# Optimization experiments

Hardware: AMD Instinct MI355X
Metric: run time of the kernel (lower is better)

The kernel has to match this reference:

```python
import jax, jax.numpy as jnp
import numpy as np
from jax import lax

NH = 8        # num_heads
C = 256       # embedding_dim
WS = 5        # window_size
DN = ('NCHW', 'OIHW', 'NCHW')


def setup_inputs() -> dict:
    key = jax.random.key(0)
    ks = jax.random.split(key, 6)
    B, H, W = 16, 64, 64
    hd = C // NH  # per-head dim = pos_embed_dim
    return {
        "src": jax.random.normal(ks[0], (B, C, H, W), jnp.float32),
        "rel_pos_embed": jax.random.normal(ks[1], (hd, WS, WS), jnp.float32) * 0.02,
        "qkv_w": jax.random.normal(ks[2], (3 * C, C), jnp.float32) * (C ** -0.5),
        "cpe_w": jax.random.normal(ks[3], (C, C, 3, 3), jnp.float32) * (1.0 / np.sqrt(C * 9)),
        "cpe_b": jnp.zeros((C,), jnp.float32),
        "out_w": jax.random.normal(ks[4], (C, C), jnp.float32) * (C ** -0.5),
        "out_b": jnp.zeros((C,), jnp.float32),
    }


def reference(src, rel_pos_embed, qkv_w, cpe_w, cpe_b, out_w, out_b):
    B, Cc, H, W = src.shape
    hd = Cc // NH
    scale = hd ** -0.5

    # conv positional encoding (3x3 conv) + residual
    x = lax.conv_general_dilated(src, cpe_w, (1, 1), [(1, 1), (1, 1)],
                                 dimension_numbers=DN) + cpe_b[None, :, None, None] + src

    # 1x1 qkv conv as a GEMM over channels
    qkv = jnp.einsum('oc,bchw->bohw', qkv_w, x)
    q, k, v = jnp.split(qkv, 3, axis=1)
    q = q.reshape(B * NH, hd, H, W)
    k = k.reshape(B * NH, hd, H, W)
    v = v.reshape(B * NH, hd, H, W)

    # linear (lambda) attention: softmax over spatial positions of k
    kf = jax.nn.softmax(k.reshape(B * NH, hd, H * W), axis=-1)   # (b' i n)
    vf = v.reshape(B * NH, hd, H * W)                            # (b' o n)
    content_lambda = jnp.einsum('bin,bon->bio', kf, vf)          # (b' i o), tiny
    qf = q.reshape(B * NH, hd, H * W) * scale
    content = jnp.einsum('bin,bio->bon', qf, content_lambda).reshape(B * NH, hd, H, W)

    # depthwise conv positional lambda on v
    pad = WS // 2
    pos_lambda = lax.conv_general_dilated(v, rel_pos_embed[:, None], (1, 1),
                                          [(pad, pad), (pad, pad)],
                                          dimension_numbers=DN,
                                          feature_group_count=hd)
    result = (content + q * pos_lambda).reshape(B, Cc, H, W)

    # 1x1 output projection
    return jnp.einsum('oc,bchw->bohw', out_w, result) + out_b[None, :, None, None]
```

## Files before the change

kernel.cpp:

```cpp
#include <hip/hip_runtime.h>


typedef unsigned short u16;
typedef __bf16 bf16x8 __attribute__((ext_vector_type(8)));
typedef float f32x4 __attribute__((ext_vector_type(4)));
#define HW 4096

__device__ __forceinline__ float bf2f(u16 u){
  unsigned v = ((unsigned)u) << 16;
  return __builtin_bit_cast(float, v);
}
__device__ __forceinline__ u16 f2bf(float f){
  unsigned u = __builtin_bit_cast(unsigned, f);
  u = u + 0x7fffu + ((u >> 16) & 1u);
  return (u16)(u >> 16);
}
__device__ __forceinline__ unsigned pack2(float a, float b){
  return (unsigned)f2bf(a) | ((unsigned)f2bf(b) << 16);
}
__device__ __forceinline__ void unpack2(unsigned u, float& a, float& b){
  a = bf2f((u16)(u & 0xffffu)); b = bf2f((u16)(u >> 16));
}
__device__ __forceinline__ void unp8(uint4 r, float* v){
  unpack2(r.x, v[0], v[1]); unpack2(r.y, v[2], v[3]);
  unpack2(r.z, v[4], v[5]); unpack2(r.w, v[6], v[7]);
}

__device__ __forceinline__ void gl2lds16(const u16* g, u16* l){
  __builtin_amdgcn_global_load_lds((__attribute__((address_space(1))) void*)g,
                                   (__attribute__((address_space(3))) void*)l, 16, 0, 0);
}

__global__ void zero_border(u16* __restrict__ xpad){
  int idx = blockIdx.x*256 + threadIdx.x;
  int g = idx & 31;
  int p = idx >> 5;
  int b = p / 260; int r = p - b*260;
  int y, x;
  if (r < 66)      { y = 0;      x = r; }
  else if (r < 132){ y = 65;     x = r-66; }
  else if (r < 196){ y = r-131;  x = 0; }
  else             { y = r-195;  x = 65; }
  *(uint4*)&xpad[((size_t)b*4356 + (size_t)y*66 + x)*256 + g*8] = uint4{0,0,0,0};
}

__global__ __launch_bounds__(256) void to_nhwc(const float* __restrict__ src,
                                               u16* __restrict__ xpad){
  __shared__ u16 sl[64*264];
  const int t = threadIdx.x, w = t>>6, lane = t&63;
  const int y = blockIdx.x, b = blockIdx.y;
  for (int cc = 0; cc < 64; ++cc){
    const int c = cc*4 + w;
    float v = src[((size_t)(b*256 + c))*HW + y*64 + lane];
    sl[lane*264 + c] = f2bf(v);
  }
  __syncthreads();
  #pragma unroll
  for (int i = 0; i < 8; ++i){
    int idx = t + 256*i;
    int p = idx >> 5, g = idx & 31;
    uint4 v = *(const uint4*)&sl[p*264 + g*8];
    *(uint4*)&xpad[((size_t)b*4356 + (size_t)(y+1)*66 + (p+1))*256 + g*8] = v;
  }
}

__global__ void repack_w(const float* __restrict__ cpe_w, const float* __restrict__ qkv_w,
                         const float* __restrict__ out_w, u16* __restrict__ wrb,
                         u16* __restrict__ wq, u16* __restrict__ wo){
  int idx = blockIdx.x*256 + threadIdx.x;
  if (idx < 589824){
    int kk = idx >> 16, o = (idx >> 8) & 255, c = idx & 255;
    wrb[idx] = f2bf(cpe_w[((o*256 + c)*9) + kk]);
  } else if (idx < 786432){
    int j = idx - 589824;
    wq[j] = f2bf(qkv_w[j]);
  } else {
    int j = idx - 786432;
    wo[j] = f2bf(out_w[j]);
  }
}

__global__ __launch_bounds__(512, 2) void conv_mfma(const u16* __restrict__ xpad,
    const u16* __restrict__ wrb, const float* __restrict__ bias,
    u16* __restrict__ xout){
  __shared__ u16 As[32768];
  __shared__ u16 Bs[32768];
  const int t = threadIdx.x, w8 = t>>6, lane = t&63;
  const int idx = blockIdx.x;
  const int nb = (idx&7)*32 + (idx>>3);
  const int pg = nb*256;
  const int b = pg>>12, row0 = (pg&4095)>>6;
  const size_t xb = (size_t)b*4356;
  const int dstb = w8*2048 + lane*8;
  const u16* aP[4]; const u16* bP[4];
  #pragma unroll
  for (int i = 0; i < 4; ++i){
    int G = (w8*4+i)*64 + lane;
    int p = G>>3, gs = (G&7) ^ (p&7);
    aP[i] = xpad + (xb + (size_t)(row0 + (p>>6) + 1)*66 + (p&63) + 1)*256 + gs*8;
    bP[i] = wrb + (size_t)p*256 + gs*8;
  }
  const int wm = w8>>2, wn = w8&3;
  const int qd = lane>>4;
  int a_off[8], b_off[4];
  #pragma unroll
  for (int m = 0; m < 8; ++m){
    int p = wm*128 + m*16 + (lane&15);
    a_off[m] = p*64 + ((qd ^ (p&7)) << 3);
  }
  #pragma unroll
  for (int n = 0; n < 4; ++n){
    int r = wn*64 + n*16 + (lane&15);
    b_off[n] = r*64 + ((qd ^ (r&7)) << 3);
  }
  f32x4 acc[8][4];
  #pragma unroll
  for (int i=0;i<8;++i)
    #pragma unroll
    for (int j=0;j<4;++j) acc[i][j] = f32x4{0.f,0.f,0.f,0.f};

  auto STAGE = [&](const int bufo, const int s){
    int c9 = s/9, tap = s - c9*9, ky = tap/3, kx = tap - ky*3;
    int offA = ((ky-1)*66 + (kx-1))*256 + c9*64;
    int offB = tap*65536 + c9*64;
    #pragma unroll
    for (int i = 0; i < 4; ++i){
      gl2lds16(aP[i] + offA, &As[bufo + dstb + i*512]);
      gl2lds16(bP[i] + offB, &Bs[bufo + dstb + i*512]);
    }
  };
  auto COMPUTE = [&](const int bufo){
    __builtin_amdgcn_s_setprio(1);
    #pragma unroll
    for (int kh = 0; kh < 2; ++kh){
      bf16x8 af[8], bfr[4];
      #pragma unroll
      for (int m = 0; m < 8; ++m)
        af[m] = __builtin_bit_cast(bf16x8, *(const uint4*)&As[bufo + (a_off[m] ^ (kh<<5))]);
      #pragma unroll
      for (int n = 0; n < 4; ++n)
        bfr[n] = __builtin_bit_cast(bf16x8, *(const uint4*)&Bs[bufo + (b_off[n] ^ (kh<<5))]);
      #pragma unroll
      for (int mt = 0; mt < 8; ++mt)
        #pragma unroll
        for (int nt = 0; nt < 4; ++nt)
          acc[mt][nt] = __builtin_amdgcn_mfma_f32_16x16x32_bf16(bfr[nt], af[mt], acc[mt][nt], 0,0,0);
    }
    __builtin_amdgcn_s_setprio(0);
  };
  #define SYNC asm volatile("s_waitcnt vmcnt(0)" ::: "memory"); __builtin_amdgcn_s_barrier();

  STAGE(0, 0);
  SYNC
  for (int s2 = 0; s2 < 18; ++s2){
    STAGE(16384, 2*s2+1);
    COMPUTE(0);
    SYNC
    if (s2 < 17) STAGE(0, 2*s2+2);
    COMPUTE(16384);
    SYNC
  }
  #pragma unroll
  for (int nt = 0; nt < 4; ++nt){
    const int och4 = wn*64 + nt*16 + qd*4;
    float4 b4 = *(const float4*)&bias[och4];
    #pragma unroll
    for (int mt = 0; mt < 8; ++mt){
      const int px = wm*128 + mt*16 + (lane&15);
      const int y = row0 + (px>>6), x = px&63;
      ushort4 r4 = *(const ushort4*)&xpad[(xb + (size_t)(y+1)*66 + x + 1)*256 + och4];
      ushort4 s;
      s.x = f2bf(acc[mt][nt][0] + b4.x + bf2f(r4.x));
      s.y = f2bf(acc[mt][nt][1] + b4.y + bf2f(r4.y));
      s.z = f2bf(acc[mt][nt][2] + b4.z + bf2f(r4.z));
      s.w = f2bf(acc[mt][nt][3] + b4.w + bf2f(r4.w));
      *(ushort4*)&xout[(size_t)(pg + px)*256 + och4] = s;
    }
  }
  #undef SYNC
}

template<int NO, int NOT, bool F32OUT>
__global__ __launch_bounds__(512, 2) void gemm_mfma(const u16* __restrict__ act,
    const u16* __restrict__ wt, const float* __restrict__ bias, void* __restrict__ out){
  __shared__ u16 As[32768];
  __shared__ u16 Bs[32768];
  const int t = threadIdx.x, w8 = t>>6, lane = t&63;
  const int idx = blockIdx.x;
  const int x8 = idx&7, q = idx>>3;
  const int ot = q % NOT, nb = x8*32 + q / NOT;
  const int pg = nb*256, o0 = ot*256;
  const int dstb = w8*2048 + lane*8;
  const u16* aP[4]; const u16* bP[4];
  #pragma unroll
  for (int i = 0; i < 4; ++i){
    int G = (w8*4+i)*64 + lane;
    int p = G>>3, gs = (G&7) ^ (p&7);
    aP[i] = act + (size_t)(pg + p)*256 + gs*8;
    bP[i] = wt  + (size_t)(o0 + p)*256 + gs*8;
  }
  const int wm = w8>>2, wn = w8&3;
  const int qd = lane>>4;
  int a_off[8], b_off[4];
  #pragma unroll
  for (int m = 0; m < 8; ++m){
    int p = wm*128 + m*16 + (lane&15);
    a_off[m] = p*64 + ((qd ^ (p&7)) << 3);
  }
  #pragma unroll
  for (int n = 0; n < 4; ++n){
    int r = wn*64 + n*16 + (lane&15);
    b_off[n] = r*64 + ((qd ^ (r&7)) << 3);
  }
  f32x4 acc[8][4];
  #pragma unroll
  for (int i=0;i<8;++i)
    #pragma unroll
    for (int j=0;j<4;++j) acc[i][j] = f32x4{0.f,0.f,0.f,0.f};

  auto STAGE = [&](const int bufo, const int s){
    const int c0 = s*64;
    #pragma unroll
    for (int i = 0; i < 4; ++i){
      gl2lds16(aP[i] + c0, &As[bufo + dstb + i*512]);
      gl2lds16(bP[i] + c0, &Bs[bufo + dstb + i*512]);
    }
  };
  auto COMPUTE = [&](const int bufo){
    __builtin_amdgcn_s_setprio(1);
    #pragma unroll
    for (int kh = 0; kh < 2; ++kh){
      bf16x8 af[8], bfr[4];
      #pragma unroll
      for (int m = 0; m < 8; ++m)
        af[m] = __builtin_bit_cast(bf16x8, *(const uint4*)&As[bufo + (a_off[m] ^ (kh<<5))]);
      #pragma unroll
      for (int n = 0; n < 4; ++n)
        bfr[n] = __builtin_bit_cast(bf16x8, *(const uint4*)&Bs[bufo + (b_off[n] ^ (kh<<5))]);
      #pragma unroll
      for (int mt = 0; mt < 8; ++mt)
        #pragma unroll
        for (int nt = 0; nt < 4; ++nt){
          if constexpr (F32OUT)
            acc[mt][nt] = __builtin_amdgcn_mfma_f32_16x16x32_bf16(af[mt], bfr[nt], acc[mt][nt], 0,0,0);
          else
            acc[mt][nt] = __builtin_amdgcn_mfma_f32_16x16x32_bf16(bfr[nt], af[mt], acc[mt][nt], 0,0,0);
        }
    }
    __builtin_amdgcn_s_setprio(0);
  };
  #define SYNC asm volatile("s_waitcnt vmcnt(0)" ::: "memory"); __builtin_amdgcn_s_barrier();

  STAGE(0, 0);
  SYNC
  for (int s2 = 0; s2 < 2; ++s2){
    STAGE(16384, 2*s2+1);
    COMPUTE(0);
    SYNC
    if (s2 < 1) STAGE(0, 2*s2+2);
    COMPUTE(16384);
    SYNC
  }
  if constexpr (F32OUT){
    const int col = lane&15, row_l = qd*4;
    const int b = pg>>12, hw0 = pg&4095;
    float* op = (float*)out;
    #pragma unroll
    for (int nt = 0; nt < 4; ++nt){
      const int och = o0 + wn*64 + nt*16 + col;
      const float bo2 = bias[och];
      #pragma unroll
      for (int mt = 0; mt < 8; ++mt){
        const int pl = wm*128 + mt*16 + row_l;
        float4 v;
        v.x = acc[mt][nt][0]+bo2; v.y = acc[mt][nt][1]+bo2;
        v.z = acc[mt][nt][2]+bo2; v.w = acc[mt][nt][3]+bo2;
        *(float4*)&op[((size_t)b*256 + och)*HW + hw0 + pl] = v;
      }
    }
  } else {
    u16* op = (u16*)out;
    #pragma unroll
    for (int nt = 0; nt < 4; ++nt){
      const int och4 = o0 + wn*64 + nt*16 + qd*4;
      #pragma unroll
      for (int mt = 0; mt < 8; ++mt){
        const int px = wm*128 + mt*16 + (lane&15);
        ushort4 s;
        s.x = f2bf(acc[mt][nt][0]); s.y = f2bf(acc[mt][nt][1]);
        s.z = f2bf(acc[mt][nt][2]); s.w = f2bf(acc[mt][nt][3]);
        *(ushort4*)&op[(size_t)(pg + px)*NO + och4] = s;
      }
    }
  }
  #undef SYNC
}

__global__ void zero_cl(float* __restrict__ cl){
  cl[blockIdx.x*256 + threadIdx.x] = 0.f;
}

__global__ __launch_bounds__(64) void lambda_kern(const u16* __restrict__ qkv,
                                                  float* __restrict__ cl,
                                                  float* __restrict__ S){
  __shared__ float Kl[64*36];
  __shared__ float Vl[64*36];
  const int t = threadIdx.x;
  const int bp = blockIdx.x, split = blockIdx.y;
  const int b = bp>>3, h = bp&7;
  const int ig = t&7, og = t>>3;
  float acc[4][4];
  float sacc[4] = {0.f,0.f,0.f,0.f};
  #pragma unroll
  for (int i=0;i<4;++i)
    #pragma unroll
    for (int j=0;j<4;++j) acc[i][j] = 0.f;
  for (int chunk = 0; chunk < 8; ++chunk){
    const int n = split*512 + chunk*64 + t;
    const u16* kp = qkv + (size_t)(b*HW + n)*768 + 256 + h*32;
    const u16* vp = kp + 256;
    uint4 k4[4], v4[4];
    #pragma unroll
    for (int qq=0;qq<4;++qq){ k4[qq] = ((const uint4*)kp)[qq]; v4[qq] = ((const uint4*)vp)[qq]; }
    __syncthreads();
    #pragma unroll
    for (int qq=0;qq<4;++qq){
      float kv[8], vv[8]; unp8(k4[qq], kv); unp8(v4[qq], vv);
      #pragma unroll
      for (int e=0;e<8;++e) kv[e] = __expf(kv[e]);
      *(float4*)&Kl[t*36 + qq*8]     = float4{kv[0],kv[1],kv[2],kv[3]};
      *(float4*)&Kl[t*36 + qq*8 + 4] = float4{kv[4],kv[5],kv[6],kv[7]};
      *(float4*)&Vl[t*36 + qq*8]     = float4{vv[0],vv[1],vv[2],vv[3]};
      *(float4*)&Vl[t*36 + qq*8 + 4] = float4{vv[4],vv[5],vv[6],vv[7]};
    }
    __syncthreads();
    for (int p = 0; p < 64; ++p){
      float4 kf = *(const float4*)&Kl[p*36 + ig*4];
      float4 vf = *(const float4*)&Vl[p*36 + og*4];
      float kfa[4] = {kf.x,kf.y,kf.z,kf.w};
      float vfa[4] = {vf.x,vf.y,vf.z,vf.w};
      #pragma unroll
      for (int i=0;i<4;++i){
        sacc[i] += kfa[i];
        #pragma unroll
        for (int j=0;j<4;++j) acc[i][j] = fmaf(kfa[i], vfa[j], acc[i][j]);
      }
    }
  }
  #pragma unroll
  for (int i=0;i<4;++i)
    #pragma unroll
    for (int j=0;j<4;++j)
      atomicAdd(&cl[(size_t)bp*1024 + (ig*4+i)*32 + og*4+j], acc[i][j]);
  if (og == 0){
    #pragma unroll
    for (int i=0;i<4;++i) atomicAdd(&S[bp*32 + ig*4 + i], sacc[i]);
  }
}

__global__ __launch_bounds__(256) void content_combine(const u16* __restrict__ qkv,
    const float* __restrict__ cl, const float* __restrict__ S,
    const float* __restrict__ rel, u16* __restrict__ res){
  __shared__ u16 vt[12800];
  __shared__ float relT[800];
  const int t = threadIdx.x;
  const int tile = blockIdx.x, h = blockIdx.y, b = blockIdx.z;
  const int x0 = (tile&3)*16, y0 = (tile>>2)*16;
  const float* __restrict__ clp = cl + (size_t)(b*8+h)*1024;
  const float* __restrict__ Sp  = S + (b*8+h)*32;
  for (int idx = t; idx < 800; idx += 256){
    int tap = idx>>5, ch = idx&31;
    relT[idx] = rel[ch*25 + tap];
  }
  #pragma unroll
  for (int i = 0; i < 7; ++i){
    int idx = t + 256*i;
    if (idx < 1600){
      int hp = idx>>2, g = idx&3;
      int hy = hp/20, hx = hp - hy*20;
      int y = y0 + hy - 2, x = x0 + hx - 2;
      uint4 v = uint4{0,0,0,0};
      if ((unsigned)y < 64u && (unsigned)x < 64u)
        v = *(const uint4*)&qkv[(size_t)(b*HW + y*64 + x)*768 + 512 + h*32 + g*8];
      *(uint4*)&vt[(g*400 + hp)*8] = v;
    }
  }
  __syncthreads();
  const int py = t>>4, px = t&15;
  const int pix = b*HW + (y0+py)*64 + x0 + px;
  const u16* qp = qkv + (size_t)pix*768 + h*32;
  float qv[32];
  {
    uint4 q0 = ((const uint4*)qp)[0], q1 = ((const uint4*)qp)[1];
    uint4 q2 = ((const uint4*)qp)[2], q3 = ((const uint4*)qp)[3];
    unp8(q0, qv); unp8(q1, qv+8); unp8(q2, qv+16); unp8(q3, qv+24);
  }
  float outv[32];
  #pragma unroll
  for (int j=0;j<32;++j) outv[j] = 0.f;
  for (int i = 0; i < 32; ++i){
    const float qi = qv[i] * 0.17677669529663687f * __builtin_amdgcn_rcpf(Sp[i]);
    #pragma unroll
    for (int g = 0; g < 8; ++g){
      float4 c4 = *(const float4*)&clp[i*32 + g*4];
      outv[g*4+0] = fmaf(qi, c4.x, outv[g*4+0]);
      outv[g*4+1] = fmaf(qi, c4.y, outv[g*4+1]);
      outv[g*4+2] = fmaf(qi, c4.z, outv[g*4+2]);
      outv[g*4+3] = fmaf(qi, c4.w, outv[g*4+3]);
    }
  }
  #pragma unroll
  for (int chg = 0; chg < 4; ++chg){
    float pos[8];
    #pragma unroll
    for (int j=0;j<8;++j) pos[j] = 0.f;
    #pragma unroll
    for (int dy = 0; dy < 5; ++dy)
      #pragma unroll
      for (int dx = 0; dx < 5; ++dx){
        int hp = (py+dy)*20 + px + dx;
        uint4 v4 = *(const uint4*)&vt[(chg*400 + hp)*8];
        float vv[8]; unp8(v4, vv);
        float4 r0 = *(const float4*)&relT[(dy*5+dx)*32 + chg*8];
        float4 r1 = *(const float4*)&relT[(dy*5+dx)*32 + chg*8 + 4];
        pos[0]=fmaf(r0.x, vv[0], pos[0]); pos[1]=fmaf(r0.y, vv[1], pos[1]);
        pos[2]=fmaf(r0.z, vv[2], pos[2]); pos[3]=fmaf(r0.w, vv[3], pos[3]);
        pos[4]=fmaf(r1.x, vv[4], pos[4]); pos[5]=fmaf(r1.y, vv[5], pos[5]);
        pos[6]=fmaf(r1.z, vv[6], pos[6]); pos[7]=fmaf(r1.w, vv[7], pos[7]);
      }
    #pragma unroll
    for (int j=0;j<8;++j) outv[chg*8+j] = fmaf(qv[chg*8+j], pos[j], outv[chg*8+j]);
  }
  u16* rp = res + (size_t)pix*256 + h*32;
  #pragma unroll
  for (int g = 0; g < 4; ++g){
    uint4 o_;
    o_.x = pack2(outv[g*8+0], outv[g*8+1]);
    o_.y = pack2(outv[g*8+2], outv[g*8+3]);
    o_.z = pack2(outv[g*8+4], outv[g*8+5]);
    o_.w = pack2(outv[g*8+6], outv[g*8+7]);
    ((uint4*)rp)[g] = o_;
  }
}

extern "C" void kernel_launch(void* const* d_in, const int* in_sizes, int n_in,
                              void* d_out, int out_size, void* d_ws, size_t ws_size,
                              hipStream_t stream) {
  const float* src   = (const float*)d_in[0];
  const float* rel   = (const float*)d_in[1];
  const float* qkv_w = (const float*)d_in[2];
  const float* cpe_w = (const float*)d_in[3];
  const float* cpe_b = (const float*)d_in[4];
  const float* out_w = (const float*)d_in[5];
  const float* out_b = (const float*)d_in[6];
  char* ws = (char*)d_ws;
  u16*   qkv  = (u16*)(ws);
  u16*   xpad = (u16*)(ws);
  u16*   xbuf = (u16*)(ws + 100663296);
  float* cl   = (float*)(ws + 134217728);
  float* S    = (float*)(ws + 134742016);
  u16*   wrb  = (u16*)(ws + 134758400);
  u16*   wq   = (u16*)(ws + 135938048);
  u16*   wo   = (u16*)(ws + 136331264);

  zero_border<<<dim3(520), dim3(256), 0, stream>>>(xpad);
  to_nhwc<<<dim3(64, 16), dim3(256), 0, stream>>>(src, xpad);
  repack_w<<<dim3(3328), dim3(256), 0, stream>>>(cpe_w, qkv_w, out_w, wrb, wq, wo);
  conv_mfma<<<dim3(256), dim3(512), 0, stream>>>(xpad, wrb, cpe_b, xbuf);
  gemm_mfma<768,3,false><<<dim3(768), dim3(512), 0, stream>>>(xbuf, wq, nullptr, (void*)qkv);
  zero_cl<<<dim3(528), dim3(256), 0, stream>>>(cl);
  lambda_kern<<<dim3(128, 8), dim3(64), 0, stream>>>(qkv, cl, S);
  content_combine<<<dim3(16, 8, 16), dim3(256), 0, stream>>>(qkv, cl, S, rel, xbuf);
  gemm_mfma<256,1,true><<<dim3(256), dim3(512), 0, stream>>>(xbuf, wo, out_b, d_out);
}
```

Baseline: 418.0 us.

## Fold content lambda into output projection weights as extra GEMM K dimension

Precomputes per-batch matrices combining out_w with the normalized content lambda, so the content term becomes a GEMM over q fused with the output projection. The combine kernel now only computes q times the positional conv, and the output GEMM runs over K=512 (q with Mb, plus q*pos with wo). This removes per-pixel 32x32 FP32 work but doubles output GEMM reads and adds a small precompute kernel plus bf16 rounding of the folded weights.

```diff
diff --git a/kernel.cpp b/kernel.cpp
--- a/kernel.cpp
+++ b/kernel.cpp
@@ -180,9 +180,9 @@
   #undef SYNC
 }
 
-template<int NO, int NOT, bool F32OUT>
+template<int NO, int NOT>
 __global__ __launch_bounds__(512, 2) void gemm_mfma(const u16* __restrict__ act,
-    const u16* __restrict__ wt, const float* __restrict__ bias, void* __restrict__ out){
+    const u16* __restrict__ wt, void* __restrict__ out){
   __shared__ u16 As[32768];
   __shared__ u16 Bs[32768];
   const int t = threadIdx.x, w8 = t>>6, lane = t&63;
@@ -240,12 +240,8 @@
       #pragma unroll
       for (int mt = 0; mt < 8; ++mt)
         #pragma unroll
-        for (int nt = 0; nt < 4; ++nt){
-          if constexpr (F32OUT)
-            acc[mt][nt] = __builtin_amdgcn_mfma_f32_16x16x32_bf16(af[mt], bfr[nt], acc[mt][nt], 0,0,0);
-          else
-            acc[mt][nt] = __builtin_amdgcn_mfma_f32_16x16x32_bf16(bfr[nt], af[mt], acc[mt][nt], 0,0,0);
-        }
+        for (int nt = 0; nt < 4; ++nt)
+          acc[mt][nt] = __builtin_amdgcn_mfma_f32_16x16x32_bf16(bfr[nt], af[mt], acc[mt][nt], 0,0,0);
     }
     __builtin_amdgcn_s_setprio(0);
   };
@@ -261,36 +257,116 @@
     COMPUTE(16384);
     SYNC
   }
-  if constexpr (F32OUT){
-    const int col = lane&15, row_l = qd*4;
-    const int b = pg>>12, hw0 = pg&4095;
-    float* op = (float*)out;
-    #pragma unroll
-    for (int nt = 0; nt < 4; ++nt){
-      const int och = o0 + wn*64 + nt*16 + col;
-      const float bo2 = bias[och];
-      #pragma unroll
-      for (int mt = 0; mt < 8; ++mt){
-        const int pl = wm*128 + mt*16 + row_l;
-        float4 v;
-        v.x = acc[mt][nt][0]+bo2; v.y = acc[mt][nt][1]+bo2;
-        v.z = acc[mt][nt][2]+bo2; v.w = acc[mt][nt][3]+bo2;
-        *(float4*)&op[((size_t)b*256 + och)*HW + hw0 + pl] = v;
-      }
-    }
-  } else {
-    u16* op = (u16*)out;
-    #pragma unroll
-    for (int nt = 0; nt < 4; ++nt){
-      const int och4 = o0 + wn*64 + nt*16 + qd*4;
-      #pragma unroll
-      for (int mt = 0; mt < 8; ++mt){
-        const int px = wm*128 + mt*16 + (lane&15);
-        ushort4 s;
-        s.x = f2bf(acc[mt][nt][0]); s.y = f2bf(acc[mt][nt][1]);
-        s.z = f2bf(acc[mt][nt][2]); s.w = f2bf(acc[mt][nt][3]);
-        *(ushort4*)&op[(size_t)(pg + px)*NO + och4] = s;
-      }
+  u16* op = (u16*)out;
+  #pragma unroll
+  for (int nt = 0; nt < 4; ++nt){
+    const int och4 = o0 + wn*64 + nt*16 + qd*4;
+    #pragma unroll
+    for (int mt = 0; mt < 8; ++mt){
+      const int px = wm*128 + mt*16 + (lane&15);
+      ushort4 s;
+      s.x = f2bf(acc[mt][nt][0]); s.y = f2bf(acc[mt][nt][1]);
+      s.z = f2bf(acc[mt][nt][2]); s.w = f2bf(acc[mt][nt][3]);
+      *(ushort4*)&op[(size_t)(pg + px)*NO + och4] = s;
+    }
+  }
+  #undef SYNC
+}
+
+__global__ __launch_bounds__(512, 2) void gemm_out(const u16* __restrict__ qkv,
+    const u16* __restrict__ qpos, const u16* __restrict__ Mb,
+    const u16* __restrict__ wo, const float* __restrict__ bias,
+    float* __restrict__ out){
+  __shared__ u16 As[32768];
+  __shared__ u16 Bs[32768];
+  const int t = threadIdx.x, w8 = t>>6, lane = t&63;
+  const int idx = blockIdx.x;
+  const int nb = (idx&7)*32 + (idx>>3);
+  const int pg = nb*256;
+  const int b = pg>>12, hw0 = pg&4095;
+  const int dstb = w8*2048 + lane*8;
+  const u16 *aQ[4], *aX[4], *bM[4], *bW[4];
+  #pragma unroll
+  for (int i = 0; i < 4; ++i){
+    int G = (w8*4+i)*64 + lane;
+    int p = G>>3, gs = (G&7) ^ (p&7);
+    aQ[i] = qkv  + (size_t)(pg + p)*768 + gs*8;
+    aX[i] = qpos + (size_t)(pg + p)*256 + gs*8;
+    bM[i] = Mb   + ((size_t)b*256 + p)*256 + gs*8;
+    bW[i] = wo   + (size_t)p*256 + gs*8;
+  }
+  const int wm = w8>>2, wn = w8&3;
+  const int qd = lane>>4;
+  int a_off[8], b_off[4];
+  #pragma unroll
+  for (int m = 0; m < 8; ++m){
+    int p = wm*128 + m*16 + (lane&15);
+    a_off[m] = p*64 + ((qd ^ (p&7)) << 3);
+  }
+  #pragma unroll
+  for (int n = 0; n < 4; ++n){
+    int r = wn*64 + n*16 + (lane&15);
+    b_off[n] = r*64 + ((qd ^ (r&7)) << 3);
+  }
+  f32x4 acc[8][4];
+  #pragma unroll
+  for (int i=0;i<8;++i)
+    #pragma unroll
+    for (int j=0;j<4;++j) acc[i][j] = f32x4{0.f,0.f,0.f,0.f};
+
+  auto STAGE = [&](const int bufo, const int s){
+    #pragma unroll
+    for (int i = 0; i < 4; ++i){
+      const u16* sa = (s < 4) ? (aQ[i] + s*64)      : (aX[i] + (s-4)*64);
+      const u16* sb = (s < 4) ? (bM[i] + s*64)      : (bW[i] + (s-4)*64);
+      gl2lds16(sa, &As[bufo + dstb + i*512]);
+      gl2lds16(sb, &Bs[bufo + dstb + i*512]);
+    }
+  };
+  auto COMPUTE = [&](const int bufo){
+    __builtin_amdgcn_s_setprio(1);
+    #pragma unroll
+    for (int kh = 0; kh < 2; ++kh){
+      bf16x8 af[8], bfr[4];
+      #pragma unroll
+      for (int m = 0; m < 8; ++m)
+        af[m] = __builtin_bit_cast(bf16x8, *(const uint4*)&As[bufo + (a_off[m] ^ (kh<<5))]);
+      #pragma unroll
+      for (int n = 0; n < 4; ++n)
+        bfr[n] = __builtin_bit_cast(bf16x8, *(const uint4*)&Bs[bufo + (b_off[n] ^ (kh<<5))]);
+      #pragma unroll
+      for (int mt = 0; mt < 8; ++mt)
+        #pragma unroll
+        for (int nt = 0; nt < 4; ++nt)
+          acc[mt][nt] = __builtin_amdgcn_mfma_f32_16x16x32_bf16(af[mt], bfr[nt], acc[mt][nt], 0,0,0);
+    }
+    __builtin_amdgcn_s_setprio(0);
+  };
+  #define SYNC asm volatile("s_waitcnt vmcnt(0)" ::: "memory"); __builtin_amdgcn_s_barrier();
+
+  STAGE(0, 0);
+  SYNC
+  #pragma unroll
+  for (int s2 = 0; s2 < 4; ++s2){
+    STAGE(16384, 2*s2+1);
+    COMPUTE(0);
+    SYNC
+    if (s2 < 3) STAGE(0, 2*s2+2);
+    COMPUTE(16384);
+    SYNC
+  }
+  const int col = lane&15, row_l = qd*4;
+  #pragma unroll
+  for (int nt = 0; nt < 4; ++nt){
+    const int och = wn*64 + nt*16 + col;
+    const float bo2 = bias[och];
+    #pragma unroll
+    for (int mt = 0; mt < 8; ++mt){
+      const int pl = wm*128 + mt*16 + row_l;
+      float4 v;
+      v.x = acc[mt][nt][0]+bo2; v.y = acc[mt][nt][1]+bo2;
+      v.z = acc[mt][nt][2]+bo2; v.w = acc[mt][nt][3]+bo2;
+      *(float4*)&out[((size_t)b*256 + och)*HW + hw0 + pl] = v;
     }
   }
   #undef SYNC
@@ -358,16 +434,42 @@
   }
 }
 
-__global__ __launch_bounds__(256) void content_combine(const u16* __restrict__ qkv,
-    const float* __restrict__ cl, const float* __restrict__ S,
+__global__ __launch_bounds__(256) void mb_kern(const float* __restrict__ cl,
+    const float* __restrict__ S, const float* __restrict__ out_w,
+    u16* __restrict__ Mb){
+  __shared__ float clS[1024];
+  __shared__ float sinv[32];
+  const int t = threadIdx.x;
+  const int h = blockIdx.x & 7, b = blockIdx.x >> 3;
+  const int bp = b*8 + h;
+  for (int idx = t; idx < 1024; idx += 256)
+    clS[idx] = cl[(size_t)bp*1024 + idx];
+  if (t < 32) sinv[t] = 0.17677669529663687f / S[bp*32 + t];
+  __syncthreads();
+  float wrow[32];
+  #pragma unroll
+  for (int o = 0; o < 32; ++o) wrow[o] = out_w[t*256 + h*32 + o];
+  u16 out16[32];
+  #pragma unroll
+  for (int i = 0; i < 32; ++i){
+    float a = 0.f;
+    #pragma unroll
+    for (int o = 0; o < 32; ++o) a = fmaf(wrow[o], clS[i*32+o], a);
+    out16[i] = f2bf(a * sinv[i]);
+  }
+  u16* mp = Mb + ((size_t)b*256 + t)*256 + h*32;
+  #pragma unroll
+  for (int g = 0; g < 4; ++g)
+    ((uint4*)mp)[g] = *(uint4*)&out16[g*8];
+}
+
+__global__ __launch_bounds__(256) void pos_combine(const u16* __restrict__ qkv,
     const float* __restrict__ rel, u16* __restrict__ res){
   __shared__ u16 vt[12800];
   __shared__ float relT[800];
   const int t = threadIdx.x;
   const int tile = blockIdx.x, h = blockIdx.y, b = blockIdx.z;
   const int x0 = (tile&3)*16, y0 = (tile>>2)*16;
-  const float* __restrict__ clp = cl + (size_t)(b*8+h)*1024;
-  const float* __restrict__ Sp  = S + (b*8+h)*32;
   for (int idx = t; idx < 800; idx += 256){
     int tap = idx>>5, ch = idx&31;
     relT[idx] = rel[ch*25 + tap];
@@ -396,19 +498,6 @@
     unp8(q0, qv); unp8(q1, qv+8); unp8(q2, qv+16); unp8(q3, qv+24);
   }
   float outv[32];
-  #pragma unroll
-  for (int j=0;j<32;++j) outv[j] = 0.f;
-  for (int i = 0; i < 32; ++i){
-    const float qi = qv[i] * 0.17677669529663687f * __builtin_amdgcn_rcpf(Sp[i]);
-    #pragma unroll
-    for (int g = 0; g < 8; ++g){
-      float4 c4 = *(const float4*)&clp[i*32 + g*4];
-      outv[g*4+0] = fmaf(qi, c4.x, outv[g*4+0]);
-      outv[g*4+1] = fmaf(qi, c4.y, outv[g*4+1]);
-      outv[g*4+2] = fmaf(qi, c4.z, outv[g*4+2]);
-      outv[g*4+3] = fmaf(qi, c4.w, outv[g*4+3]);
-    }
-  }
   #pragma unroll
   for (int chg = 0; chg < 4; ++chg){
     float pos[8];
@@ -429,7 +518,7 @@
         pos[6]=fmaf(r1.z, vv[6], pos[6]); pos[7]=fmaf(r1.w, vv[7], pos[7]);
       }
     #pragma unroll
-    for (int j=0;j<8;++j) outv[chg*8+j] = fmaf(qv[chg*8+j], pos[j], outv[chg*8+j]);
+    for (int j=0;j<8;++j) outv[chg*8+j] = qv[chg*8+j] * pos[j];
   }
   u16* rp = res + (size_t)pix*256 + h*32;
   #pragma unroll
@@ -461,15 +550,17 @@
   float* S    = (float*)(ws + 134742016);
   u16*   wrb  = (u16*)(ws + 134758400);
   u16*   wq   = (u16*)(ws + 135938048);
-  u16*   wo   = (u16*)(ws + 136331264);
+  u16*   Mb   = (u16*)(ws + 134758400);
+  u16*   wo   = (u16*)(ws + 136855552);
 
   zero_border<<<dim3(520), dim3(256), 0, stream>>>(xpad);
   to_nhwc<<<dim3(64, 16), dim3(256), 0, stream>>>(src, xpad);
   repack_w<<<dim3(3328), dim3(256), 0, stream>>>(cpe_w, qkv_w, out_w, wrb, wq, wo);
   conv_mfma<<<dim3(256), dim3(512), 0, stream>>>(xpad, wrb, cpe_b, xbuf);
-  gemm_mfma<768,3,false><<<dim3(768), dim3(512), 0, stream>>>(xbuf, wq, nullptr, (void*)qkv);
+  gemm_mfma<768,3><<<dim3(768), dim3(512), 0, stream>>>(xbuf, wq, (void*)qkv);
   zero_cl<<<dim3(528), dim3(256), 0, stream>>>(cl);
   lambda_kern<<<dim3(128, 8), dim3(64), 0, stream>>>(qkv, cl, S);
-  content_combine<<<dim3(16, 8, 16), dim3(256), 0, stream>>>(qkv, cl, S, rel, xbuf);
-  gemm_mfma<256,1,true><<<dim3(256), dim3(512), 0, stream>>>(xbuf, wo, out_b, d_out);
-}
+  mb_kern<<<dim3(128), dim3(256), 0, stream>>>(cl, S, out_w, Mb);
+  pos_combine<<<dim3(16, 8, 16), dim3(256), 0, stream>>>(qkv, rel, xbuf);
+  gemm_out<<<dim3(256), dim3(512), 0, stream>>>(qkv, xbuf, Mb, wo, out_b, (float*)d_out);
+}
```

Result: no change. 413.7 us (-1.0%).
